# Kernel tuning notes

Measured on AMD Instinct MI355X. Metric: run time of the kernel, lower is better.

The kernel has to match this reference:

```python
import jax, jax.numpy as jnp
import numpy as np

INPUT_SIZE = 1024
HIDDEN_SIZE = 2048
BATCH = 4096


def _xavier(key, shape):
    fan_out, fan_in = shape
    std = jnp.sqrt(2.0 / (fan_in + fan_out)).astype(jnp.float32)
    return jax.random.normal(key, shape, dtype=jnp.float32) * std


def setup_inputs() -> dict:
    key = jax.random.key(0)
    ks = jax.random.split(key, 8)
    return {
        "x": jax.random.normal(ks[0], (BATCH, INPUT_SIZE), dtype=jnp.float32),
        "hprev": jax.random.normal(ks[1], (BATCH, HIDDEN_SIZE), dtype=jnp.float32),
        "Wh": _xavier(ks[2], (HIDDEN_SIZE, INPUT_SIZE)),
        "Wz": _xavier(ks[3], (HIDDEN_SIZE, INPUT_SIZE)),
        "Wr": _xavier(ks[4], (HIDDEN_SIZE, INPUT_SIZE)),
        "Uh": _xavier(ks[5], (HIDDEN_SIZE, HIDDEN_SIZE)),
        "Uz": _xavier(ks[6], (HIDDEN_SIZE, HIDDEN_SIZE)),
        "Ur": _xavier(ks[7], (HIDDEN_SIZE, HIDDEN_SIZE)),
        "bh": jnp.zeros((HIDDEN_SIZE,), dtype=jnp.float32),
        "bz": jnp.zeros((HIDDEN_SIZE,), dtype=jnp.float32),
        "br": jnp.zeros((HIDDEN_SIZE,), dtype=jnp.float32),
    }


def reference(x, hprev, Wh, Wz, Wr, Uh, Uz, Ur, bh, bz, br):
    # batched matvec: (b,i) @ (h,i)^T -> (b,h)
    r = jax.nn.sigmoid(x @ Wr.T + hprev @ Ur.T + br)
    z = jax.nn.sigmoid(x @ Wz.T + hprev @ Uz.T + bz)
    h_proposed = jnp.tanh(x @ Wh.T + (r * hprev) @ Uh.T + bh)
    return z * h_proposed + (1.0 - z) * hprev
```

## Files before the change

kernel.cpp:

```cpp
#include <hip/hip_runtime.h>

#define BATCH 4096
#define ISZ   1024
#define HSZ   2048

typedef __bf16 bf16x8 __attribute__((ext_vector_type(8)));
typedef float  f32x4  __attribute__((ext_vector_type(4)));

__device__ __forceinline__ unsigned short f2bf(float f) {
  unsigned u = __builtin_bit_cast(unsigned, f);
  u += 0x7fffu + ((u >> 16) & 1u);
  return (unsigned short)(u >> 16);
}
__device__ __forceinline__ float bf2f(unsigned short s) {
  unsigned u = ((unsigned)s) << 16;
  return __builtin_bit_cast(float, u);
}

struct CvtArgs {
  const float* src[6];
  unsigned short* dst[6];
  int cum[7];
};

__global__ __launch_bounds__(256) void cvt_all_kernel(CvtArgs a, int total4) {
  int i = blockIdx.x * 256 + threadIdx.x;
  if (i >= total4) return;
  int s = 0;
#pragma unroll
  for (int k = 0; k < 5; ++k) s += (i >= a.cum[k + 1]) ? 1 : 0;
  int off = i - a.cum[s];
  float4 f = ((const float4*)a.src[s])[off];
  ushort4 o;
  o.x = f2bf(f.x); o.y = f2bf(f.y); o.z = f2bf(f.z); o.w = f2bf(f.w);
  ((ushort4*)a.dst[s])[off] = o;
}

__device__ __forceinline__ void stage_tile64(const unsigned short* __restrict__ g, int ldK,
                                             int tileRow, int k0, char* lds, int t) {
  char* l0 = lds + ((t >> 6) << 10);
#pragma unroll
  for (int k = 0; k < 4; ++k) {
    int linear = t + k * 256;
    int row = linear >> 3;
    int cs  = linear & 7;
    int c   = cs ^ (row & 7);
    const unsigned short* gp = g + (size_t)(tileRow + row) * ldK + (k0 + c * 8);
    __builtin_amdgcn_global_load_lds((const __attribute__((address_space(1))) void*)gp,
                                     (__attribute__((address_space(3))) void*)(l0 + k * 4096),
                                     16, 0, 0);
  }
}

__device__ __forceinline__ void stage_tile64_w8(const unsigned short* __restrict__ g, int ldK,
                                                int tileRow, int k0, char* lds, int t) {
  char* l0 = lds + ((t >> 6) << 10);
#pragma unroll
  for (int k = 0; k < 2; ++k) {
    int linear = t + k * 512;
    int row = linear >> 3;
    int cs  = linear & 7;
    int c   = cs ^ (row & 7);
    const unsigned short* gp = g + (size_t)(tileRow + row) * ldK + (k0 + c * 8);
    __builtin_amdgcn_global_load_lds((const __attribute__((address_space(1))) void*)gp,
                                     (__attribute__((address_space(3))) void*)(l0 + k * 8192),
                                     16, 0, 0);
  }
}

__device__ __forceinline__ void gemm_seg_rz(const unsigned short* __restrict__ A,
                                            const unsigned short* __restrict__ Br,
                                            const unsigned short* __restrict__ Bz,
                                            int K, int rowBase, int colBase,
                                            char* ldsA, char* ldsBr, char* ldsBz,
                                            f32x4 (&accR)[4][4], f32x4 (&accZ)[4][4], int t) {
  const int lane = t & 63;
  const int wid  = t >> 6;
  const int wm   = wid >> 1, wn = wid & 1;
  const int lrow = lane & 15;
  const int quad = lane >> 4;
  const int r7   = lrow & 7;
  for (int k0 = 0; k0 < K; k0 += 64) {
    stage_tile64(A,  K, rowBase, k0, ldsA,  t);
    stage_tile64(Br, K, colBase, k0, ldsBr, t);
    stage_tile64(Bz, K, colBase, k0, ldsBz, t);
    __syncthreads();
#pragma unroll
    for (int kk = 0; kk < 2; ++kk) {
      const int swz = (((kk << 2) | quad) ^ r7) * 16;
      bf16x8 af[4], bfr[4];
#pragma unroll
      for (int i = 0; i < 4; ++i)
        af[i] = *(const bf16x8*)(ldsA + (wm * 64 + i * 16 + lrow) * 128 + swz);
#pragma unroll
      for (int j = 0; j < 4; ++j)
        bfr[j] = *(const bf16x8*)(ldsBr + (wn * 64 + j * 16 + lrow) * 128 + swz);
#pragma unroll
      for (int i = 0; i < 4; ++i)
#pragma unroll
        for (int j = 0; j < 4; ++j)
          accR[i][j] = __builtin_amdgcn_mfma_f32_16x16x32_bf16(af[i], bfr[j], accR[i][j], 0, 0, 0);
#pragma unroll
      for (int j = 0; j < 4; ++j)
        bfr[j] = *(const bf16x8*)(ldsBz + (wn * 64 + j * 16 + lrow) * 128 + swz);
#pragma unroll
      for (int i = 0; i < 4; ++i)
#pragma unroll
        for (int j = 0; j < 4; ++j)
          accZ[i][j] = __builtin_amdgcn_mfma_f32_16x16x32_bf16(af[i], bfr[j], accZ[i][j], 0, 0, 0);
    }
    __syncthreads();
  }
}

__device__ __forceinline__ void gemm_seg8(const unsigned short* __restrict__ A,
                                          const unsigned short* __restrict__ W,
                                          int K, int rowBase, int colBase,
                                          char* ldsA, char* ldsB,
                                          f32x4 (&acc)[4][2], int t) {
  const int lane = t & 63;
  const int wid  = t >> 6;
  const int wm   = wid >> 2;
  const int wn   = wid & 3;
  const int lrow = lane & 15;
  const int quad = lane >> 4;
  const int r7   = lrow & 7;
  for (int k0 = 0; k0 < K; k0 += 64) {
    stage_tile64_w8(A, K, rowBase, k0, ldsA, t);
    stage_tile64_w8(W, K, colBase, k0, ldsB, t);
    __syncthreads();
#pragma unroll
    for (int kk = 0; kk < 2; ++kk) {
      const int swz = (((kk << 2) | quad) ^ r7) * 16;
      bf16x8 af[4], bfr[2];
#pragma unroll
      for (int i = 0; i < 4; ++i)
        af[i]  = *(const bf16x8*)(ldsA + (wm * 64 + i * 16 + lrow) * 128 + swz);
#pragma unroll
      for (int j = 0; j < 2; ++j)
        bfr[j] = *(const bf16x8*)(ldsB + (wn * 32 + j * 16 + lrow) * 128 + swz);
#pragma unroll
      for (int i = 0; i < 4; ++i)
#pragma unroll
        for (int j = 0; j < 2; ++j)
          acc[i][j] = __builtin_amdgcn_mfma_f32_16x16x32_bf16(af[i], bfr[j], acc[i][j], 0, 0, 0);
    }
    __syncthreads();
  }
}

__device__ __forceinline__ float fast_sigmoid(float v) {
  return 1.0f / (1.0f + __expf(-v));
}
__device__ __forceinline__ float fast_tanh(float v) {
  float e = __expf(2.0f * v);
  return 1.0f - 2.0f / (e + 1.0f);
}

__global__ __launch_bounds__(256, 2) void gate_rz(
    const unsigned short* __restrict__ xb, const unsigned short* __restrict__ hb,
    const unsigned short* __restrict__ Wr, const unsigned short* __restrict__ Ur,
    const unsigned short* __restrict__ Wz, const unsigned short* __restrict__ Uz,
    const float* __restrict__ br, const float* __restrict__ bz,
    const float* __restrict__ Wh32, const float* __restrict__ Uh32,
    unsigned short* __restrict__ Whb, unsigned short* __restrict__ Uhb,
    unsigned short* __restrict__ rh, unsigned short* __restrict__ Zbuf) {
  __shared__ char lds[49152];
  const int t = threadIdx.x;

  if (blockIdx.z == 0) {
    const int NW = (HSZ * ISZ) / 4;
    const int NU = (HSZ * HSZ) / 4;
    int tid = (blockIdx.x + (blockIdx.y << 4)) * 256 + t;
    for (int i = tid; i < NW + NU; i += 512 * 256) {
      const float4* s4 = (i < NW) ? (const float4*)Wh32 + i
                                  : (const float4*)Uh32 + (i - NW);
      ushort4* d4 = (i < NW) ? (ushort4*)Whb + i
                             : (ushort4*)Uhb + (i - NW);
      float4 f = *s4;
      ushort4 o;
      o.x = f2bf(f.x); o.y = f2bf(f.y); o.z = f2bf(f.z); o.w = f2bf(f.w);
      *d4 = o;
    }
    return;
  }

  char* ldsA  = lds;
  char* ldsBr = lds + 16384;
  char* ldsBz = lds + 32768;

  int lin = blockIdx.x + (blockIdx.y << 4);
  int xcd = lin & 7, s = lin >> 3;
  int bx = xcd * 2 + (s & 1);
  int by = s >> 1;

  const int rowBase = by * 128;
  const int colBase = bx * 128;

  f32x4 accR[4][4], accZ[4][4];
#pragma unroll
  for (int i = 0; i < 4; ++i)
#pragma unroll
    for (int j = 0; j < 4; ++j) {
      accR[i][j] = (f32x4){0.f, 0.f, 0.f, 0.f};
      accZ[i][j] = (f32x4){0.f, 0.f, 0.f, 0.f};
    }

  gemm_seg_rz(xb, Wr, Wz, ISZ, rowBase, colBase, ldsA, ldsBr, ldsBz, accR, accZ, t);
  gemm_seg_rz(hb, Ur, Uz, HSZ, rowBase, colBase, ldsA, ldsBr, ldsBz, accR, accZ, t);

  const int lane = t & 63, wid = t >> 6;
  const int wm = wid >> 1, wn = wid & 1, lrow = lane & 15, quad = lane >> 4;
#pragma unroll
  for (int i = 0; i < 4; ++i) {
#pragma unroll
    for (int j = 0; j < 4; ++j) {
      int col = colBase + wn * 64 + j * 16 + lrow;
      float bvr = br[col];
      float bvz = bz[col];
#pragma unroll
      for (int r = 0; r < 4; ++r) {
        int row = rowBase + wm * 64 + i * 16 + quad * 4 + r;
        int idx = row * HSZ + col;
        float hv = bf2f(hb[idx]);
        float sr = fast_sigmoid(accR[i][j][r] + bvr);
        float sz = fast_sigmoid(accZ[i][j][r] + bvz);
        rh[idx]   = f2bf(sr * hv);
        Zbuf[idx] = f2bf(sz);
      }
    }
  }
}

__global__ __launch_bounds__(512, 4) void gate_h(
    const unsigned short* __restrict__ xb, const unsigned short* __restrict__ rhb,
    const unsigned short* __restrict__ Wh, const unsigned short* __restrict__ Uh,
    const float* __restrict__ bh, const unsigned short* __restrict__ Zbuf,
    const float* __restrict__ hprev, float* __restrict__ out) {
  __shared__ char lds[32768];
  char* ldsA = lds;
  char* ldsB = lds + 16384;
  const int t = threadIdx.x;

  int lin = blockIdx.x + (blockIdx.y << 4);
  int xcd = lin & 7, s = lin >> 3;
  int bx = xcd * 2 + (s & 1);
  int by = s >> 1;

  const int rowBase = by * 128;
  const int colBase = bx * 128;

  f32x4 acc[4][2];
#pragma unroll
  for (int i = 0; i < 4; ++i)
#pragma unroll
    for (int j = 0; j < 2; ++j)
      acc[i][j] = (f32x4){0.f, 0.f, 0.f, 0.f};

  gemm_seg8(xb, Wh, ISZ, rowBase, colBase, ldsA, ldsB, acc, t);
  gemm_seg8(rhb, Uh, HSZ, rowBase, colBase, ldsA, ldsB, acc, t);

  const int lane = t & 63, wid = t >> 6;
  const int wm = wid >> 2, wn = wid & 3, lrow = lane & 15, quad = lane >> 4;
#pragma unroll
  for (int i = 0; i < 4; ++i) {
#pragma unroll
    for (int j = 0; j < 2; ++j) {
      int col = colBase + wn * 32 + j * 16 + lrow;
      float bv = bh[col];
#pragma unroll
      for (int r = 0; r < 4; ++r) {
        int row = rowBase + wm * 64 + i * 16 + quad * 4 + r;
        float hp = fast_tanh(acc[i][j][r] + bv);
        int idx = row * HSZ + col;
        float z = bf2f(Zbuf[idx]);
        float h = hprev[idx];
        out[idx] = h + z * (hp - h);
      }
    }
  }
}

extern "C" void kernel_launch(void* const* d_in, const int* in_sizes, int n_in,
                              void* d_out, int out_size, void* d_ws, size_t ws_size,
                              hipStream_t stream) {
  (void)in_sizes; (void)n_in; (void)out_size; (void)ws_size;
  const float* x     = (const float*)d_in[0];
  const float* hprev = (const float*)d_in[1];
  const float* Wh    = (const float*)d_in[2];
  const float* Wz    = (const float*)d_in[3];
  const float* Wr    = (const float*)d_in[4];
  const float* Uh    = (const float*)d_in[5];
  const float* Uz    = (const float*)d_in[6];
  const float* Ur    = (const float*)d_in[7];
  const float* bh    = (const float*)d_in[8];
  const float* bz    = (const float*)d_in[9];
  const float* br    = (const float*)d_in[10];
  float* out = (float*)d_out;

  char* ws = (char*)d_ws;
  size_t off = 0;
  auto alloc = [&](size_t bytes) { char* p = ws + off; off += bytes; return p; };
  unsigned short* xb  = (unsigned short*)alloc((size_t)BATCH * ISZ * 2);
  unsigned short* hb  = (unsigned short*)alloc((size_t)BATCH * HSZ * 2);
  unsigned short* Wrb = (unsigned short*)alloc((size_t)HSZ * ISZ * 2);
  unsigned short* Wzb = (unsigned short*)alloc((size_t)HSZ * ISZ * 2);
  unsigned short* Whb = (unsigned short*)alloc((size_t)HSZ * ISZ * 2);
  unsigned short* Urb = (unsigned short*)alloc((size_t)HSZ * HSZ * 2);
  unsigned short* Uzb = (unsigned short*)alloc((size_t)HSZ * HSZ * 2);
  unsigned short* Uhb = (unsigned short*)alloc((size_t)HSZ * HSZ * 2);
  unsigned short* rhb = (unsigned short*)alloc((size_t)BATCH * HSZ * 2);
  unsigned short* Zb  = (unsigned short*)alloc((size_t)BATCH * HSZ * 2);

  CvtArgs ca;
  const float* srcs[6]      = {x, hprev, Wr, Wz, Ur, Uz};
  unsigned short* dsts[6]   = {xb, hb, Wrb, Wzb, Urb, Uzb};
  int n4s[6] = {BATCH * ISZ / 4, BATCH * HSZ / 4,
                HSZ * ISZ / 4, HSZ * ISZ / 4,
                HSZ * HSZ / 4, HSZ * HSZ / 4};
  int cum = 0;
  for (int i = 0; i < 6; ++i) {
    ca.src[i] = srcs[i];
    ca.dst[i] = dsts[i];
    ca.cum[i] = cum;
    cum += n4s[i];
  }
  ca.cum[6] = cum;
  cvt_all_kernel<<<(cum + 255) / 256, 256, 0, stream>>>(ca, cum);

  dim3 gridA(HSZ / 128, BATCH / 128, 2);
  gate_rz<<<gridA, 256, 0, stream>>>(xb, hb, Wrb, Urb, Wzb, Uzb, br, bz,
                                     Wh, Uh, Whb, Uhb, rhb, Zb);

  dim3 gridB(HSZ / 128, BATCH / 128, 1);
  gate_h<<<gridB, 512, 0, stream>>>(xb, rhb, Whb, Uhb, bh, Zb, hprev, out);
}
```

Baseline: 328.9 us.

## Widen gate_h tile to 128x256 reusing dual-B GEMM routine

Replaces the 128x128, 512-thread gate_h tiling with a 128x256 tile per 256-thread block, reusing the two-B-matrix segment routine from the r/z gate. Each A tile is loaded once and multiplied against two adjacent 128-column weight slices. The aim is to raise arithmetic intensity and cut A-operand traffic. In exchange the grid halves to one block per CU, per-block occupancy drops, and the XCD-aware block remapping is removed.

```diff
diff --git a/kernel.cpp b/kernel.cpp
--- a/kernel.cpp
+++ b/kernel.cpp
@@ -48,22 +48,6 @@
     const unsigned short* gp = g + (size_t)(tileRow + row) * ldK + (k0 + c * 8);
     __builtin_amdgcn_global_load_lds((const __attribute__((address_space(1))) void*)gp,
                                      (__attribute__((address_space(3))) void*)(l0 + k * 4096),
-                                     16, 0, 0);
-  }
-}
-
-__device__ __forceinline__ void stage_tile64_w8(const unsigned short* __restrict__ g, int ldK,
-                                                int tileRow, int k0, char* lds, int t) {
-  char* l0 = lds + ((t >> 6) << 10);
-#pragma unroll
-  for (int k = 0; k < 2; ++k) {
-    int linear = t + k * 512;
-    int row = linear >> 3;
-    int cs  = linear & 7;
-    int c   = cs ^ (row & 7);
-    const unsigned short* gp = g + (size_t)(tileRow + row) * ldK + (k0 + c * 8);
-    __builtin_amdgcn_global_load_lds((const __attribute__((address_space(1))) void*)gp,
-                                     (__attribute__((address_space(3))) void*)(l0 + k * 8192),
                                      16, 0, 0);
   }
 }
@@ -113,42 +97,6 @@
   }
 }
 
-__device__ __forceinline__ void gemm_seg8(const unsigned short* __restrict__ A,
-                                          const unsigned short* __restrict__ W,
-                                          int K, int rowBase, int colBase,
-                                          char* ldsA, char* ldsB,
-                                          f32x4 (&acc)[4][2], int t) {
-  const int lane = t & 63;
-  const int wid  = t >> 6;
-  const int wm   = wid >> 2;
-  const int wn   = wid & 3;
-  const int lrow = lane & 15;
-  const int quad = lane >> 4;
-  const int r7   = lrow & 7;
-  for (int k0 = 0; k0 < K; k0 += 64) {
-    stage_tile64_w8(A, K, rowBase, k0, ldsA, t);
-    stage_tile64_w8(W, K, colBase, k0, ldsB, t);
-    __syncthreads();
-#pragma unroll
-    for (int kk = 0; kk < 2; ++kk) {
-      const int swz = (((kk << 2) | quad) ^ r7) * 16;
-      bf16x8 af[4], bfr[2];
-#pragma unroll
-      for (int i = 0; i < 4; ++i)
-        af[i]  = *(const bf16x8*)(ldsA + (wm * 64 + i * 16 + lrow) * 128 + swz);
-#pragma unroll
-      for (int j = 0; j < 2; ++j)
-        bfr[j] = *(const bf16x8*)(ldsB + (wn * 32 + j * 16 + lrow) * 128 + swz);
-#pragma unroll
-      for (int i = 0; i < 4; ++i)
-#pragma unroll
-        for (int j = 0; j < 2; ++j)
-          acc[i][j] = __builtin_amdgcn_mfma_f32_16x16x32_bf16(af[i], bfr[j], acc[i][j], 0, 0, 0);
-    }
-    __syncthreads();
-  }
-}
-
 __device__ __forceinline__ float fast_sigmoid(float v) {
   return 1.0f / (1.0f + __expf(-v));
 }
@@ -232,53 +180,58 @@
   }
 }
 
-__global__ __launch_bounds__(512, 4) void gate_h(
+__global__ __launch_bounds__(256, 2) void gate_h(
     const unsigned short* __restrict__ xb, const unsigned short* __restrict__ rhb,
     const unsigned short* __restrict__ Wh, const unsigned short* __restrict__ Uh,
     const float* __restrict__ bh, const unsigned short* __restrict__ Zbuf,
     const float* __restrict__ hprev, float* __restrict__ out) {
-  __shared__ char lds[32768];
-  char* ldsA = lds;
-  char* ldsB = lds + 16384;
+  __shared__ char lds[49152];
+  char* ldsA  = lds;
+  char* ldsB0 = lds + 16384;
+  char* ldsB1 = lds + 32768;
   const int t = threadIdx.x;
 
-  int lin = blockIdx.x + (blockIdx.y << 4);
-  int xcd = lin & 7, s = lin >> 3;
-  int bx = xcd * 2 + (s & 1);
-  int by = s >> 1;
-
-  const int rowBase = by * 128;
-  const int colBase = bx * 128;
-
-  f32x4 acc[4][2];
+  const int colBase = blockIdx.x * 256;
+  const int rowBase = blockIdx.y * 128;
+
+  f32x4 accL[4][4], accR2[4][4];
 #pragma unroll
   for (int i = 0; i < 4; ++i)
 #pragma unroll
-    for (int j = 0; j < 2; ++j)
-      acc[i][j] = (f32x4){0.f, 0.f, 0.f, 0.f};
-
-  gemm_seg8(xb, Wh, ISZ, rowBase, colBase, ldsA, ldsB, acc, t);
-  gemm_seg8(rhb, Uh, HSZ, rowBase, colBase, ldsA, ldsB, acc, t);
+    for (int j = 0; j < 4; ++j) {
+      accL[i][j]  = (f32x4){0.f, 0.f, 0.f, 0.f};
+      accR2[i][j] = (f32x4){0.f, 0.f, 0.f, 0.f};
+    }
+
+  gemm_seg_rz(xb,  Wh, Wh + (size_t)128 * ISZ, ISZ, rowBase, colBase,
+              ldsA, ldsB0, ldsB1, accL, accR2, t);
+  gemm_seg_rz(rhb, Uh, Uh + (size_t)128 * HSZ, HSZ, rowBase, colBase,
+              ldsA, ldsB0, ldsB1, accL, accR2, t);
 
   const int lane = t & 63, wid = t >> 6;
-  const int wm = wid >> 2, wn = wid & 3, lrow = lane & 15, quad = lane >> 4;
-#pragma unroll
-  for (int i = 0; i < 4; ++i) {
-#pragma unroll
-    for (int j = 0; j < 2; ++j) {
-      int col = colBase + wn * 32 + j * 16 + lrow;
-      float bv = bh[col];
-#pragma unroll
-      for (int r = 0; r < 4; ++r) {
-        int row = rowBase + wm * 64 + i * 16 + quad * 4 + r;
-        float hp = fast_tanh(acc[i][j][r] + bv);
-        int idx = row * HSZ + col;
-        float z = bf2f(Zbuf[idx]);
-        float h = hprev[idx];
-        out[idx] = h + z * (hp - h);
+  const int wm = wid >> 1, wn = wid & 1, lrow = lane & 15, quad = lane >> 4;
+
+  auto epi = [&](f32x4 (&acc)[4][4], int colOff) {
+#pragma unroll
+    for (int i = 0; i < 4; ++i) {
+#pragma unroll
+      for (int j = 0; j < 4; ++j) {
+        int col = colBase + colOff + wn * 64 + j * 16 + lrow;
+        float bv = bh[col];
+#pragma unroll
+        for (int r = 0; r < 4; ++r) {
+          int row = rowBase + wm * 64 + i * 16 + quad * 4 + r;
+          float hp = fast_tanh(acc[i][j][r] + bv);
+          int idx = row * HSZ + col;
+          float z = bf2f(Zbuf[idx]);
+          float h = hprev[idx];
+          out[idx] = h + z * (hp - h);
+        }
       }
     }
-  }
+  };
+  epi(accL, 0);
+  epi(accR2, 128);
 }
 
 extern "C" void kernel_launch(void* const* d_in, const int* in_sizes, int n_in,
@@ -332,6 +285,6 @@
   gate_rz<<<gridA, 256, 0, stream>>>(xb, hb, Wrb, Urb, Wzb, Uzb, br, bz,
                                      Wh, Uh, Whb, Uhb, rhb, Zb);
 
-  dim3 gridB(HSZ / 128, BATCH / 128, 1);
-  gate_h<<<gridB, 512, 0, stream>>>(xb, rhb, Whb, Uhb, bh, Zb, hprev, out);
-}
+  dim3 gridB(8, BATCH / 128, 1);
+  gate_h<<<gridB, 256, 0, stream>>>(xb, rhb, Whb, Uhb, bh, Zb, hprev, out);
+}
```

Measured after the change: 356.0 us. +8.2%, slower.
